# Optimization experiments

Measured on AMD Instinct MI355X. Metric: run time of the kernel, lower is better.

## Reference

```python
import jax, jax.numpy as jnp
import numpy as np
import math

B, S = 4, 1024
V, D, L, H, F, MAXLEN = 32000, 1024, 6, 16, 4096, 2048
DH = D // H
NUM_BUCKETS, MAX_DIST = 32, 256
REL_SCALE = 64.0 ** 0.5
EPS = 1e-5


def setup_inputs() -> dict:
    key = jax.random.key(0)
    ks = iter(jax.random.split(key, 32))
    sd = 0.02
    inp = {
        'src': jax.random.randint(next(ks), (B, S), 0, V),
        'src_mask': jnp.ones((B, 1, 1, S), dtype=jnp.int32),
        'tok_emb': jax.random.normal(next(ks), (V, D), jnp.float32) * sd,
        'pos_emb': jax.random.normal(next(ks), (MAXLEN, D), jnp.float32) * sd,
        'Wq': jax.random.normal(next(ks), (L, D, D), jnp.float32) * sd,
        'bq': jnp.zeros((L, D), jnp.float32),
        'Wk': jax.random.normal(next(ks), (L, D, D), jnp.float32) * sd,
        'bk': jnp.zeros((L, D), jnp.float32),
        'Wv': jax.random.normal(next(ks), (L, D, D), jnp.float32) * sd,
        'bv': jnp.zeros((L, D), jnp.float32),
        'Wo': jax.random.normal(next(ks), (L, D, D), jnp.float32) * sd,
        'bo': jnp.zeros((L, D), jnp.float32),
        'rel_bias': jax.random.normal(next(ks), (L, NUM_BUCKETS, H), jnp.float32) * sd,
        'ln1_g': jnp.ones((L, D), jnp.float32),
        'ln1_b': jnp.zeros((L, D), jnp.float32),
        'W1': jax.random.normal(next(ks), (L, D, F), jnp.float32) * sd,
        'b1': jnp.zeros((L, F), jnp.float32),
        'W2': jax.random.normal(next(ks), (L, F, D), jnp.float32) * sd,
        'b2': jnp.zeros((L, D), jnp.float32),
        'ln2_g': jnp.ones((L, D), jnp.float32),
        'ln2_b': jnp.zeros((L, D), jnp.float32),
    }
    return inp


def _rel_pos_bucket(seq_len):
    # non-causal bucketing (T5-style), matching the torch source
    q = jnp.arange(seq_len)
    k = jnp.arange(seq_len)
    n = q[:, None] - k[None, :]          # == -(k - q)
    nb = NUM_BUCKETS // 2                # 16
    ret = (n < 0).astype(jnp.int32) * nb
    n = jnp.abs(n)
    max_exact = nb // 2                  # 8
    is_small = n < max_exact
    val_large = max_exact + (
        jnp.log(jnp.maximum(n, 1).astype(jnp.float32) / max_exact)
        / math.log(MAX_DIST / max_exact) * (nb - max_exact)
    ).astype(jnp.int32)
    val_large = jnp.minimum(val_large, nb - 1)
    return ret + jnp.where(is_small, n, val_large)  # [S,S] in [0,32)


def _layer_norm(x, g, b):
    mu = jnp.mean(x, axis=-1, keepdims=True)
    var = jnp.var(x, axis=-1, keepdims=True)
    return (x - mu) * jax.lax.rsqrt(var + EPS) * g + b


def reference(src, src_mask, tok_emb, pos_emb, Wq, bq, Wk, bk, Wv, bv, Wo, bo,
              rel_bias, ln1_g, ln1_b, W1, b1, W2, b2, ln2_g, ln2_b):
    seq_len = src.shape[1]
    bucket = _rel_pos_bucket(seq_len)                      # [S,S] int
    x = tok_emb[src] * jnp.sqrt(jnp.float32(D)) + pos_emb[jnp.arange(seq_len)][None]
    scale = jnp.sqrt(jnp.float32(DH))
    neg = jnp.float32(-1e10)

    def layer(x, p):
        (wq, bq_, wk, bk_, wv, bv_, wo, bo_, rb, g1, b1_, w1, bb1, w2, bb2, g2, b2_) = p
        Q = (x @ wq + bq_).reshape(B, seq_len, H, DH)
        K = (x @ wk + bk_).reshape(B, seq_len, H, DH)
        Vv = (x @ wv + bv_).reshape(B, seq_len, H, DH)
        energy = jnp.einsum('bqhd,bkhd->bhqk', Q, K) / scale
        energy = jnp.where(src_mask == 0, neg, energy)
        bias = rb[bucket]                                  # [S,S,H]
        energy = energy + jnp.transpose(bias, (2, 0, 1))[None] * REL_SCALE
        attn = jax.nn.softmax(energy, axis=-1)
        o = jnp.einsum('bhqk,bkhd->bqhd', attn, Vv).reshape(B, seq_len, D)
        o = o @ wo + bo_
        x = _layer_norm(x + o, g1, b1_)
        f = jax.nn.relu(x @ w1 + bb1) @ w2 + bb2
        x = _layer_norm(x + f, g2, b2_)
        return x, None

    params = (Wq, bq, Wk, bk, Wv, bv, Wo, bo, rel_bias,
              ln1_g, ln1_b, W1, b1, W2, b2, ln2_g, ln2_b)
    x, _ = jax.lax.scan(layer, x, params)
    return x
```

## Files before the change

kernel.cpp:

```cpp
#include <hip/hip_runtime.h>

#define B_ 4
#define S_ 1024
#define D_ 1024
#define F_ 4096
#define H_ 16
#define L_ 6
#define M_ (B_*S_)

typedef unsigned short u16;
typedef __attribute__((ext_vector_type(4))) unsigned short u16x4;
typedef __attribute__((ext_vector_type(8))) short s16x8;
typedef __attribute__((ext_vector_type(8))) __bf16 bf16x8;
typedef __attribute__((ext_vector_type(4))) float f32x4;

typedef const __attribute__((address_space(1))) unsigned int gu32;
typedef __attribute__((address_space(3))) unsigned int su32;

__device__ __forceinline__ u16 f2bf(float f) {
  union { float f; unsigned u; } v; v.f = f;
  unsigned u = v.u;
  return (u16)((u + 0x7fffu + ((u >> 16) & 1u)) >> 16);
}

__device__ __forceinline__ f32x4 mfma16(s16x8 a, s16x8 b, f32x4 c) {
  return __builtin_amdgcn_mfma_f32_16x16x32_bf16(
      __builtin_bit_cast(bf16x8, a), __builtin_bit_cast(bf16x8, b), c, 0, 0, 0);
}

__device__ __forceinline__ void gload16(const void* g, void* s) {
  __builtin_amdgcn_global_load_lds((gu32*)g, (su32*)s, 16, 0, 0);
}

template<int OUTMODE>
__device__ __forceinline__ void gemm128_body(
    const u16* __restrict__ A, const u16* __restrict__ Bt,
    const float* __restrict__ bias, float* __restrict__ Cf,
    u16* __restrict__ Ch, int N, int K, int kbeg, int kend,
    const float* __restrict__ bias2, const float* __restrict__ bias3)
{
  __shared__ __align__(16) u16 As[128 * 64];
  __shared__ __align__(16) u16 Bs[128 * 64];
  const int tid = threadIdx.x, lane = tid & 63, w = tid >> 6;
  const int bm = blockIdx.x * 128, bn = blockIdx.y * 128;
  const int wm = (w >> 1) * 64, wn = (w & 1) * 64;

  f32x4 acc[4][4];
#pragma unroll
  for (int i = 0; i < 4; i++)
#pragma unroll
    for (int j = 0; j < 4; j++) acc[i][j] = {0.f, 0.f, 0.f, 0.f};

  for (int k0 = kbeg; k0 < kend; k0 += 64) {
    __syncthreads();
#pragma unroll
    for (int i = 0; i < 4; i++) {
      const int flat = i * 4096 + w * 1024 + lane * 16;
      const int row = flat >> 7, ce = (flat & 127) >> 1;
      gload16(A + (size_t)(bm + row) * K + k0 + ce, As + i * 2048 + w * 512);
      gload16(Bt + (size_t)(bn + row) * K + k0 + ce, Bs + i * 2048 + w * 512);
    }
    __syncthreads();
#pragma unroll
    for (int kk = 0; kk < 2; kk++) {
      s16x8 af[4], bf[4];
#pragma unroll
      for (int mf = 0; mf < 4; mf++)
        af[mf] = *(const s16x8*)&As[(wm + mf * 16 + (lane & 15)) * 64 + kk * 32 + (lane >> 4) * 8];
#pragma unroll
      for (int nf = 0; nf < 4; nf++)
        bf[nf] = *(const s16x8*)&Bs[(wn + nf * 16 + (lane & 15)) * 64 + kk * 32 + (lane >> 4) * 8];
#pragma unroll
      for (int mf = 0; mf < 4; mf++)
#pragma unroll
        for (int nf = 0; nf < 4; nf++)
          acc[mf][nf] = mfma16(af[mf], bf[nf], acc[mf][nf]);
    }
  }
#pragma unroll
  for (int nf = 0; nf < 4; nf++) {
    const int col = bn + wn + nf * 16 + (lane & 15);
    float bvv = 0.f, sc = 1.0f;
    int zz = 0, lc = col;
    if (OUTMODE == 3) {
      zz = col >> 10; lc = col & 1023;
      const float* bp = (zz == 0) ? bias : (zz == 1) ? bias2 : bias3;
      bvv = bp[lc];
      sc = (zz == 0) ? 0.125f : 1.0f;
    }
#pragma unroll
    for (int mf = 0; mf < 4; mf++) {
#pragma unroll
      for (int j = 0; j < 4; j++) {
        const int row = bm + wm + mf * 16 + ((lane >> 4) << 2) + j;
        const float v = acc[mf][nf][j];
        if (OUTMODE == 0) {
          Cf[(size_t)row * N + col] = v;
        } else {
          Ch[(size_t)zz * M_ * D_ + (size_t)row * D_ + lc] = f2bf((v + bvv) * sc);
        }
      }
    }
  }
}

__global__ __launch_bounds__(256, 3) void gemm_qkvf(
    const u16* __restrict__ A, const u16* __restrict__ WT,
    const float* __restrict__ bq, const float* __restrict__ bk,
    const float* __restrict__ bv, u16* __restrict__ Out)
{
  gemm128_body<3>(A, WT, bq, nullptr, Out, 3 * D_, D_, 0, D_, bk, bv);
}

__global__ __launch_bounds__(256, 3) void gemm_splitk2(
    const u16* __restrict__ A, const u16* __restrict__ WT,
    float* __restrict__ P, int N, int K)
{
  const int z = blockIdx.z;
  const int half = K >> 1;
  gemm128_body<0>(A, WT, nullptr, P + (size_t)z * M_ * (size_t)N, nullptr,
                  N, K, z * half, z * half + half, nullptr, nullptr);
}

__device__ __forceinline__ s16x8 readfrag(const u16* half, int r, int kk, int hi4) {
  const int c = (kk * 64 + hi4 * 16) ^ ((r & 7) << 4);
  return *(const s16x8*)((const char*)half + r * 128 + c);
}

__device__ __forceinline__ void stage_half(
    const u16* __restrict__ src, int ldk, u16* lds_half, int w, int lane)
{
#pragma unroll
  for (int j = 0; j < 2; j++) {
    const int flat = j * 8192 + w * 1024 + lane * 16;
    const int row = flat >> 7;
    const int kb = (flat & 127) ^ ((row & 7) << 4);
    gload16(src + (size_t)row * ldk + (kb >> 1), lds_half + j * 4096 + w * 512);
  }
}

#define BAR     asm volatile("s_barrier" ::: "memory")
#define PH_PRE  asm volatile("s_barrier" ::: "memory"); __builtin_amdgcn_s_setprio(1)
#define PH_POST __builtin_amdgcn_s_setprio(0); __builtin_amdgcn_sched_barrier(0)
#define VM4     asm volatile("s_waitcnt vmcnt(4)" ::: "memory")
#define VM0     asm volatile("s_waitcnt vmcnt(0)" ::: "memory")

#define READ_B(bufhalf) do { \
  _Pragma("unroll") for (int nf = 0; nf < 4; nf++) \
  _Pragma("unroll") for (int kk = 0; kk < 2; kk++) \
    bfr[nf][kk] = readfrag(bufhalf, rb0 + nf * 16 + lo16, kk, hi4); } while (0)
#define READ_A(bufhalf, Q) do { \
  _Pragma("unroll") for (int m = 0; m < 2; m++) \
  _Pragma("unroll") for (int kk = 0; kk < 2; kk++) \
    af[m][kk] = readfrag(bufhalf, (2 * (Q) + m) * 16 + lo16, kk, hi4); } while (0)
#define DO_MFMA(Q) do { \
  _Pragma("unroll") for (int kk = 0; kk < 2; kk++) \
  _Pragma("unroll") for (int m = 0; m < 2; m++) \
  _Pragma("unroll") for (int nf = 0; nf < 4; nf++) \
    acc[2 * (Q) + m][nf] = mfma16(af[m][kk], bfr[nf][kk], acc[2 * (Q) + m][nf]); } while (0)

__global__ __launch_bounds__(512, 2) void gemm_ffn1(
    const u16* __restrict__ A, const u16* __restrict__ Bt,
    const float* __restrict__ bias, u16* __restrict__ Ch)
{
  __shared__ __align__(16) u16 As[2][2][8192];
  __shared__ __align__(16) u16 Bs[2][2][8192];
  const int tid = threadIdx.x, lane = tid & 63, w = tid >> 6;
  const int wr = w >> 2, wc = w & 3;
  const int lo16 = lane & 15, hi4 = lane >> 4;
  const int bm = blockIdx.x * 256, bn = blockIdx.y * 256;
  const int rb0 = (wc & 1) * 64;
  const int K = D_, N = F_;

  const u16* Abase = A + (size_t)bm * K;
  const u16* Bbase = Bt + (size_t)bn * K;
  const size_t h1 = (size_t)128 * K;
  const int NT = K >> 6, NI = NT >> 1;

  f32x4 acc[8][4];
#pragma unroll
  for (int i = 0; i < 8; i++)
#pragma unroll
    for (int j = 0; j < 4; j++) acc[i][j] = {0.f, 0.f, 0.f, 0.f};

  stage_half(Abase,           K, As[0][0], w, lane);
  stage_half(Abase + h1,      K, As[0][1], w, lane);
  stage_half(Bbase,           K, Bs[0][0], w, lane);
  stage_half(Bbase + h1,      K, Bs[0][1], w, lane);
  stage_half(Abase + 64,      K, As[1][0], w, lane);
  stage_half(Abase + h1 + 64, K, As[1][1], w, lane);
  stage_half(Bbase + 64,      K, Bs[1][0], w, lane);
  stage_half(Bbase + h1 + 64, K, Bs[1][1], w, lane);
  asm volatile("s_waitcnt vmcnt(8)" ::: "memory");
  BAR;

  const u16* Ae = As[0][wr]; const u16* Ao = As[1][wr];
  const u16* Be = Bs[0][wc >> 1]; const u16* Bo = Bs[1][wc >> 1];
  s16x8 af[2][2], bfr[4][2];

  for (int it = 0; it < NI - 1; ++it) {
    READ_B(Be); READ_A(Ae, 0);
    if (it > 0) {
      stage_half(Abase +      (size_t)(2 * it + 1) * 64, K, As[1][0], w, lane);
      stage_half(Abase + h1 + (size_t)(2 * it + 1) * 64, K, As[1][1], w, lane);
    }
    PH_PRE; DO_MFMA(0); PH_POST; BAR;
    READ_A(Ae, 1);
    stage_half(Bbase +      (size_t)(2 * it + 2) * 64, K, Bs[0][0], w, lane);
    PH_PRE; DO_MFMA(1); PH_POST; BAR;
    READ_A(Ae, 2);
    stage_half(Bbase + h1 + (size_t)(2 * it + 2) * 64, K, Bs[0][1], w, lane);
    PH_PRE; DO_MFMA(2); PH_POST; BAR;
    READ_A(Ae, 3);
    PH_PRE; DO_MFMA(3); PH_POST; VM4; BAR;
    READ_B(Bo); READ_A(Ao, 0);
    stage_half(Abase +      (size_t)(2 * it + 2) * 64, K, As[0][0], w, lane);
    stage_half(Abase + h1 + (size_t)(2 * it + 2) * 64, K, As[0][1], w, lane);
    PH_PRE; DO_MFMA(0); PH_POST; BAR;
    READ_A(Ao, 1);
    stage_half(Bbase +      (size_t)(2 * it + 3) * 64, K, Bs[1][0], w, lane);
    PH_PRE; DO_MFMA(1); PH_POST; BAR;
    READ_A(Ao, 2);
    stage_half(Bbase + h1 + (size_t)(2 * it + 3) * 64, K, Bs[1][1], w, lane);
    PH_PRE; DO_MFMA(2); PH_POST; BAR;
    READ_A(Ao, 3);
    PH_PRE; DO_MFMA(3); PH_POST; VM4; BAR;
  }
  READ_B(Be); READ_A(Ae, 0);
  stage_half(Abase +      (size_t)(NT - 1) * 64, K, As[1][0], w, lane);
  stage_half(Abase + h1 + (size_t)(NT - 1) * 64, K, As[1][1], w, lane);
  PH_PRE; DO_MFMA(0); PH_POST; BAR;
  READ_A(Ae, 1);             PH_PRE; DO_MFMA(1); PH_POST; BAR;
  READ_A(Ae, 2);             PH_PRE; DO_MFMA(2); PH_POST; BAR;
  READ_A(Ae, 3);             PH_PRE; DO_MFMA(3); PH_POST; VM0; BAR;
  READ_B(Bo); READ_A(Ao, 0); PH_PRE; DO_MFMA(0); PH_POST; BAR;
  READ_A(Ao, 1);             PH_PRE; DO_MFMA(1); PH_POST; BAR;
  READ_A(Ao, 2);             PH_PRE; DO_MFMA(2); PH_POST; BAR;
  READ_A(Ao, 3);             PH_PRE; DO_MFMA(3); PH_POST;

  const int row0 = bm + wr * 128, col0 = bn + wc * 64;
#pragma unroll
  for (int nf = 0; nf < 4; nf++) {
    const int col = col0 + nf * 16 + lo16;
    const float bv = bias[col];
#pragma unroll
    for (int mf = 0; mf < 8; mf++) {
#pragma unroll
      for (int j = 0; j < 4; j++) {
        const int row = row0 + mf * 16 + hi4 * 4 + j;
        Ch[(size_t)row * N + col] = f2bf(fmaxf(acc[mf][nf][j] + bv, 0.f));
      }
    }
  }
}

__global__ __launch_bounds__(256) void transpose_cvt(
    const float* __restrict__ src, u16* __restrict__ dst, int R, int Cc)
{
  __shared__ float t[32][33];
  const int c0 = blockIdx.x * 32, r0 = blockIdx.y * 32;
  const int tx = threadIdx.x & 31, ty = threadIdx.x >> 5;
#pragma unroll
  for (int i = 0; i < 4; i++)
    t[ty + 8 * i][tx] = src[(size_t)(r0 + ty + 8 * i) * Cc + c0 + tx];
  __syncthreads();
#pragma unroll
  for (int i = 0; i < 4; i++)
    dst[(size_t)(c0 + ty + 8 * i) * R + r0 + tx] = f2bf(t[tx][ty + 8 * i]);
}

__global__ __launch_bounds__(256) void transpose4(
    const float* __restrict__ Wq, const float* __restrict__ Wk,
    const float* __restrict__ Wv, const float* __restrict__ Wo,
    u16* __restrict__ WTqkv, u16* __restrict__ WTo)
{
  __shared__ float t[32][33];
  const int z = blockIdx.z;
  const float* src = (z == 0) ? Wq : (z == 1) ? Wk : (z == 2) ? Wv : Wo;
  u16* dst = (z < 3) ? WTqkv + (size_t)z * D_ * D_ : WTo;
  const int c0 = blockIdx.x * 32, r0 = blockIdx.y * 32;
  const int tx = threadIdx.x & 31, ty = threadIdx.x >> 5;
#pragma unroll
  for (int i = 0; i < 4; i++)
    t[ty + 8 * i][tx] = src[(size_t)(r0 + ty + 8 * i) * D_ + c0 + tx];
  __syncthreads();
#pragma unroll
  for (int i = 0; i < 4; i++)
    dst[(size_t)(c0 + ty + 8 * i) * D_ + r0 + tx] = f2bf(t[tx][ty + 8 * i]);
}

__global__ __launch_bounds__(256) void vt_transpose(
    const u16* __restrict__ Vb, u16* __restrict__ Vt)
{
  __shared__ u16 t[64][66];
  const int s0 = blockIdx.x * 64;
  const int bh = blockIdx.y;
  const int b = bh >> 4, h = bh & 15;
  const int tid = threadIdx.x;
  const int row = tid >> 2;
  const int c0 = (tid & 3) * 16;
  const u16* src = Vb + (size_t)(b * S_ + s0 + row) * D_ + h * 64 + c0;
  *(s16x8*)&t[row][c0] = *(const s16x8*)src;
  *(s16x8*)&t[row][c0 + 8] = *(const s16x8*)(src + 8);
  __syncthreads();
  const int dh = tid >> 2;
  const int sc = (tid & 3) * 16;
  s16x8 a, bv;
#pragma unroll
  for (int u = 0; u < 8; u++) a[u] = (short)t[sc + u][dh];
#pragma unroll
  for (int u = 0; u < 8; u++) bv[u] = (short)t[sc + 8 + u][dh];
  u16* dst = Vt + (size_t)(bh * 64 + dh) * S_ + s0 + sc;
  *(s16x8*)dst = a;
  *(s16x8*)(dst + 8) = bv;
}

__device__ __forceinline__ s16x8 lds_swz(const u16* base, int row, int cb) {
  const int addr = row * 128 + (cb ^ ((row & 7) << 4));
  return *(const s16x8*)((const char*)base + addr);
}

__global__ __launch_bounds__(256, 4) void attn_kernel(
    const u16* __restrict__ Qb, const u16* __restrict__ Kb,
    const u16* __restrict__ Vt, const int* __restrict__ mask,
    const float* __restrict__ rb, u16* __restrict__ AO)
{
  __shared__ float lut[2048];
  __shared__ __align__(16) u16 Ks[64 * 64];
  __shared__ __align__(16) u16 Vs[64 * 64];
  __shared__ __align__(16) u16 Ps[4][16 * 68];

  const int tid = threadIdx.x;
  const int lane = tid & 63;
  const int w = tid >> 6;
  const int bh = blockIdx.x;
  const int b = bh >> 4, h = bh & 15;
  const int q0 = blockIdx.y * 64 + w * 16;
  const int bS = b * S_, hh = h * 64;

  for (int idx = tid; idx < 2048; idx += 256) {
    const int rel = idx - 1024;
    const int ret = rel < 0 ? 16 : 0;
    const int n = rel < 0 ? -rel : rel;
    int bu;
    if (n < 8) bu = ret + n;
    else {
      const float t = logf((float)n * 0.125f) * (8.0f / 3.4657359027997265f);
      int vl = 8 + (int)t;
      if (vl > 15) vl = 15;
      bu = ret + vl;
    }
    lut[idx] = rb[bu * 16 + h] * 8.0f;
  }

  s16x8 qf[2];
#pragma unroll
  for (int kk = 0; kk < 2; kk++)
    qf[kk] = *(const s16x8*)(Qb + (size_t)(bS + q0 + (lane & 15)) * D_ + hh +
                             kk * 32 + (lane >> 4) * 8);

  f32x4 oacc[4];
#pragma unroll
  for (int i = 0; i < 4; i++) oacc[i] = {0.f, 0.f, 0.f, 0.f};
  float rm[4], rl[4];
#pragma unroll
  for (int j = 0; j < 4; j++) { rm[j] = -3e38f; rl[j] = 0.f; }

  for (int kt = 0; kt < S_; kt += 64) {
    __syncthreads();
#pragma unroll
    for (int i = 0; i < 2; i++) {
      const int flat = i * 4096 + w * 1024 + lane * 16;
      const int row = flat >> 7;
      const int ce = ((flat & 127) ^ ((row & 7) << 4)) >> 1;
      gload16(Kb + (size_t)(bS + kt + row) * D_ + hh + ce, Ks + i * 2048 + w * 512);
      gload16(Vt + (size_t)(bh * 64 + row) * S_ + kt + ce, Vs + i * 2048 + w * 512);
    }
    __syncthreads();

    f32x4 sacc[4];
#pragma unroll
    for (int i = 0; i < 4; i++) sacc[i] = {0.f, 0.f, 0.f, 0.f};
#pragma unroll
    for (int kk = 0; kk < 2; kk++) {
      const int cb = kk * 64 + (lane >> 4) * 16;
#pragma unroll
      for (int nf = 0; nf < 4; nf++) {
        const s16x8 kb = lds_swz(Ks, nf * 16 + (lane & 15), cb);
        sacc[nf] = mfma16(qf[kk], kb, sacc[nf]);
      }
    }

    int km[4];
#pragma unroll
    for (int nf = 0; nf < 4; nf++)
      km[nf] = mask[bS + kt + nf * 16 + (lane & 15)];

    const int lidx0 = q0 + (lane >> 4) * 4 + 1024 - kt - (lane & 15);
#pragma unroll
    for (int j = 0; j < 4; j++) {
      const int lrow = ((lane >> 4) << 2) + j;
      float sc[4];
      float mx = -3e38f;
#pragma unroll
      for (int nf = 0; nf < 4; nf++) {
        float s = (km[nf] == 0) ? -1e10f : sacc[nf][j];
        s += lut[lidx0 + j - nf * 16];
        sc[nf] = s;
        mx = fmaxf(mx, s);
      }
      mx = fmaxf(mx, __shfl_xor(mx, 1));
      mx = fmaxf(mx, __shfl_xor(mx, 2));
      mx = fmaxf(mx, __shfl_xor(mx, 4));
      mx = fmaxf(mx, __shfl_xor(mx, 8));
      const float m_new = fmaxf(rm[j], mx);
      const float fs = __expf(rm[j] - m_new);
      rm[j] = m_new;
      float psum = 0.f;
#pragma unroll
      for (int nf = 0; nf < 4; nf++) {
        const float p = __expf(sc[nf] - m_new);
        psum += p;
        Ps[w][lrow * 68 + nf * 16 + (lane & 15)] = f2bf(p);
      }
      psum += __shfl_xor(psum, 1);
      psum += __shfl_xor(psum, 2);
      psum += __shfl_xor(psum, 4);
      psum += __shfl_xor(psum, 8);
      rl[j] = rl[j] * fs + psum;
#pragma unroll
      for (int df = 0; df < 4; df++) oacc[df][j] *= fs;
    }

#pragma unroll
    for (int kk = 0; kk < 2; kk++) {
      const s16x8 pa = *(const s16x8*)&Ps[w][(lane & 15) * 68 + kk * 32 + (lane >> 4) * 8];
      const int cb = kk * 64 + (lane >> 4) * 16;
#pragma unroll
      for (int df = 0; df < 4; df++) {
        const s16x8 vb = lds_swz(Vs, df * 16 + (lane & 15), cb);
        oacc[df] = mfma16(pa, vb, oacc[df]);
      }
    }
  }

  float inv[4];
#pragma unroll
  for (int j = 0; j < 4; j++) inv[j] = 1.0f / rl[j];
#pragma unroll
  for (int df = 0; df < 4; df++)
#pragma unroll
    for (int j = 0; j < 4; j++) {
      const int qrow = q0 + ((lane >> 4) << 2) + j;
      AO[(size_t)(bS + qrow) * D_ + hh + df * 16 + (lane & 15)] =
          f2bf(oacc[df][j] * inv[j]);
    }
}

__global__ __launch_bounds__(256) void ln_fused2(
    const float* __restrict__ X, const float* __restrict__ P0,
    const float* __restrict__ P1, const float* __restrict__ bias,
    const float* __restrict__ g, const float* __restrict__ be,
    float* __restrict__ Yf, u16* __restrict__ Yh)
{
  const int row = blockIdx.x;
  const int tid = threadIdx.x;
  const size_t off = (size_t)row * D_;
  const float4 xv = ((const float4*)(X + off))[tid];
  const float4 p0 = ((const float4*)(P0 + off))[tid];
  const float4 p1 = ((const float4*)(P1 + off))[tid];
  const float4 bb = ((const float4*)bias)[tid];
  const float v0 = xv.x + p0.x + p1.x + bb.x;
  const float v1 = xv.y + p0.y + p1.y + bb.y;
  const float v2 = xv.z + p0.z + p1.z + bb.z;
  const float v3 = xv.w + p0.w + p1.w + bb.w;
  float sum = v0 + v1 + v2 + v3;
  float ss = v0 * v0 + v1 * v1 + v2 * v2 + v3 * v3;
#pragma unroll
  for (int o = 1; o < 64; o <<= 1) {
    sum += __shfl_xor(sum, o);
    ss += __shfl_xor(ss, o);
  }
  __shared__ float s1[4], s2[4];
  if ((tid & 63) == 0) { s1[tid >> 6] = sum; s2[tid >> 6] = ss; }
  __syncthreads();
  sum = s1[0] + s1[1] + s1[2] + s1[3];
  ss = s2[0] + s2[1] + s2[2] + s2[3];
  const float mu = sum * (1.f / D_);
  const float var = ss * (1.f / D_) - mu * mu;
  const float rstd = rsqrtf(var + 1e-5f);
  const float4 gv = ((const float4*)g)[tid];
  const float4 bv = ((const float4*)be)[tid];
  float4 y;
  y.x = (v0 - mu) * rstd * gv.x + bv.x;
  y.y = (v1 - mu) * rstd * gv.y + bv.y;
  y.z = (v2 - mu) * rstd * gv.z + bv.z;
  y.w = (v3 - mu) * rstd * gv.w + bv.w;
  ((float4*)(Yf + off))[tid] = y;
  u16x4 hv;
  hv.x = f2bf(y.x); hv.y = f2bf(y.y); hv.z = f2bf(y.z); hv.w = f2bf(y.w);
  ((u16x4*)(Yh + off))[tid] = hv;
}

__global__ __launch_bounds__(256) void embed_kernel(
    const int* __restrict__ src, const float* __restrict__ tok,
    const float* __restrict__ pos, float* __restrict__ X, u16* __restrict__ Xh)
{
  const int row = blockIdx.x;
  const int s = row & (S_ - 1);
  const int t = src[row];
  const int tid = threadIdx.x;
  const float4 tv = ((const float4*)(tok + (size_t)t * D_))[tid];
  const float4 pv = ((const float4*)(pos + (size_t)s * D_))[tid];
  float4 y;
  y.x = tv.x * 32.f + pv.x;
  y.y = tv.y * 32.f + pv.y;
  y.z = tv.z * 32.f + pv.z;
  y.w = tv.w * 32.f + pv.w;
  ((float4*)(X + (size_t)row * D_))[tid] = y;
  u16x4 hv;
  hv.x = f2bf(y.x); hv.y = f2bf(y.y); hv.z = f2bf(y.z); hv.w = f2bf(y.w);
  ((u16x4*)(Xh + (size_t)row * D_))[tid] = hv;
}

extern "C" void kernel_launch(void* const* d_in, const int* in_sizes, int n_in,
                              void* d_out, int out_size, void* d_ws, size_t ws_size,
                              hipStream_t stream)
{
  const int* src = (const int*)d_in[0];
  const int* mask = (const int*)d_in[1];
  const float* tok_emb = (const float*)d_in[2];
  const float* pos_emb = (const float*)d_in[3];
  const float* Wq = (const float*)d_in[4];
  const float* bq = (const float*)d_in[5];
  const float* Wk = (const float*)d_in[6];
  const float* bk = (const float*)d_in[7];
  const float* Wv = (const float*)d_in[8];
  const float* bv = (const float*)d_in[9];
  const float* Wo = (const float*)d_in[10];
  const float* bo = (const float*)d_in[11];
  const float* rb = (const float*)d_in[12];
  const float* g1 = (const float*)d_in[13];
  const float* b1n = (const float*)d_in[14];
  const float* W1 = (const float*)d_in[15];
  const float* b1f = (const float*)d_in[16];
  const float* W2 = (const float*)d_in[17];
  const float* b2f = (const float*)d_in[18];
  const float* g2 = (const float*)d_in[19];
  const float* b2n = (const float*)d_in[20];
  float* out = (float*)d_out;

  char* ws = (char*)d_ws;
  const size_t MB = 1ull << 20;
  float* xb   = (float*)(ws + 0);
  u16*   xb16 = (u16*)(ws + 16 * MB);
  u16*   Qb16 = (u16*)(ws + 24 * MB);
  u16*   Kb16 = (u16*)(ws + 32 * MB);
  u16*   Vb16 = (u16*)(ws + 40 * MB);
  u16*   Vt16 = (u16*)(ws + 48 * MB);
  u16*   AO16 = (u16*)(ws + 56 * MB);
  float* Pp   = (float*)(ws + 64 * MB);
  u16*   WTqkv= (u16*)(ws + 96 * MB);
  u16*   WTo  = (u16*)(ws + 102 * MB);
  u16*   WT1  = (u16*)(ws + 104 * MB);
  u16*   WT2  = (u16*)(ws + 112 * MB);
  u16*   Hb16 = (u16*)(ws + 24 * MB);

  embed_kernel<<<M_, 256, 0, stream>>>(src, tok_emb, pos_emb, xb, xb16);

  for (int l = 0; l < L_; l++) {
    const size_t oDD = (size_t)l * D_ * D_;
    const size_t oDF = (size_t)l * D_ * F_;

    transpose4<<<dim3(32, 32, 4), 256, 0, stream>>>(
        Wq + oDD, Wk + oDD, Wv + oDD, Wo + oDD, WTqkv, WTo);
    transpose_cvt<<<dim3(F_ / 32, D_ / 32), 256, 0, stream>>>(W1 + oDF, WT1, D_, F_);
    transpose_cvt<<<dim3(D_ / 32, F_ / 32), 256, 0, stream>>>(W2 + oDF, WT2, F_, D_);

    gemm_qkvf<<<dim3(M_ / 128, 3 * D_ / 128), 256, 0, stream>>>(
        xb16, WTqkv, bq + l * D_, bk + l * D_, bv + l * D_, Qb16);

    vt_transpose<<<dim3(S_ / 64, B_ * H_), 256, 0, stream>>>(Vb16, Vt16);

    attn_kernel<<<dim3(B_ * H_, S_ / 64), 256, 0, stream>>>(
        Qb16, Kb16, Vt16, mask, rb + l * 32 * H_, AO16);

    gemm_splitk2<<<dim3(M_ / 128, D_ / 128, 2), 256, 0, stream>>>(
        AO16, WTo, Pp, D_, D_);

    ln_fused2<<<M_, 256, 0, stream>>>(
        xb, Pp, Pp + (size_t)M_ * D_, bo + l * D_,
        g1 + l * D_, b1n + l * D_, xb, xb16);

    gemm_ffn1<<<dim3(M_ / 256, F_ / 256), 512, 0, stream>>>(
        xb16, WT1, b1f + l * F_, Hb16);

    gemm_splitk2<<<dim3(M_ / 128, D_ / 128, 2), 256, 0, stream>>>(
        Hb16, WT2, Pp, D_, F_);

    ln_fused2<<<M_, 256, 0, stream>>>(
        xb, Pp, Pp + (size_t)M_ * D_, b2f + l * D_,
        g2 + l * D_, b2n + l * D_, (l == L_ - 1) ? out : xb, xb16);
  }
}
```

Before: 1.515 ms.

## Use bf16 residual and split-K partials, 256-tile FFN2, double-buffer attention KV

```diff
diff --git a/kernel.cpp b/kernel.cpp
--- a/kernel.cpp
+++ b/kernel.cpp
@@ -22,6 +22,9 @@
   unsigned u = v.u;
   return (u16)((u + 0x7fffu + ((u >> 16) & 1u)) >> 16);
 }
+__device__ __forceinline__ float bf2f(u16 h) {
+  union { unsigned u; float f; } v; v.u = (unsigned)h << 16; return v.f;
+}
 
 __device__ __forceinline__ f32x4 mfma16(s16x8 a, s16x8 b, f32x4 c) {
   return __builtin_amdgcn_mfma_f32_16x16x32_bf16(
@@ -35,9 +38,9 @@
 template<int OUTMODE>
 __device__ __forceinline__ void gemm128_body(
     const u16* __restrict__ A, const u16* __restrict__ Bt,
-    const float* __restrict__ bias, float* __restrict__ Cf,
-    u16* __restrict__ Ch, int N, int K, int kbeg, int kend,
-    const float* __restrict__ bias2, const float* __restrict__ bias3)
+    const float* __restrict__ b0, const float* __restrict__ b1,
+    const float* __restrict__ b2, u16* __restrict__ Ch,
+    int N, int K, int kbeg, int kend)
 {
   __shared__ __align__(16) u16 As[128 * 64];
   __shared__ __align__(16) u16 Bs[128 * 64];
@@ -84,7 +87,7 @@
     int zz = 0, lc = col;
     if (OUTMODE == 3) {
       zz = col >> 10; lc = col & 1023;
-      const float* bp = (zz == 0) ? bias : (zz == 1) ? bias2 : bias3;
+      const float* bp = (zz == 0) ? b0 : (zz == 1) ? b1 : b2;
       bvv = bp[lc];
       sc = (zz == 0) ? 0.125f : 1.0f;
     }
@@ -94,8 +97,8 @@
       for (int j = 0; j < 4; j++) {
         const int row = bm + wm + mf * 16 + ((lane >> 4) << 2) + j;
         const float v = acc[mf][nf][j];
-        if (OUTMODE == 0) {
-          Cf[(size_t)row * N + col] = v;
+        if (OUTMODE == 1) {
+          Ch[(size_t)row * N + col] = f2bf(v);
         } else {
           Ch[(size_t)zz * M_ * D_ + (size_t)row * D_ + lc] = f2bf((v + bvv) * sc);
         }
@@ -109,17 +112,16 @@
     const float* __restrict__ bq, const float* __restrict__ bk,
     const float* __restrict__ bv, u16* __restrict__ Out)
 {
-  gemm128_body<3>(A, WT, bq, nullptr, Out, 3 * D_, D_, 0, D_, bk, bv);
-}
-
-__global__ __launch_bounds__(256, 3) void gemm_splitk2(
+  gemm128_body<3>(A, WT, bq, bk, bv, Out, 3 * D_, D_, 0, D_);
+}
+
+__global__ __launch_bounds__(256, 3) void gemm_osplit2(
     const u16* __restrict__ A, const u16* __restrict__ WT,
-    float* __restrict__ P, int N, int K)
+    u16* __restrict__ P)
 {
   const int z = blockIdx.z;
-  const int half = K >> 1;
-  gemm128_body<0>(A, WT, nullptr, P + (size_t)z * M_ * (size_t)N, nullptr,
-                  N, K, z * half, z * half + half, nullptr, nullptr);
+  gemm128_body<1>(A, WT, nullptr, nullptr, nullptr,
+                  P + (size_t)z * M_ * D_, D_, D_, z * 512, z * 512 + 512);
 }
 
 __device__ __forceinline__ s16x8 readfrag(const u16* half, int r, int kk, int hi4) {
@@ -159,9 +161,11 @@
   _Pragma("unroll") for (int nf = 0; nf < 4; nf++) \
     acc[2 * (Q) + m][nf] = mfma16(af[m][kk], bfr[nf][kk], acc[2 * (Q) + m][nf]); } while (0)
 
-__global__ __launch_bounds__(512, 2) void gemm_ffn1(
+template<int OUTMODE>
+__device__ __forceinline__ void gemm256_body(
     const u16* __restrict__ A, const u16* __restrict__ Bt,
-    const float* __restrict__ bias, u16* __restrict__ Ch)
+    const float* __restrict__ bias, u16* __restrict__ Ch,
+    int N, int K, int kbeg, int kslice)
 {
   __shared__ __align__(16) u16 As[2][2][8192];
   __shared__ __align__(16) u16 Bs[2][2][8192];
@@ -170,12 +174,11 @@
   const int lo16 = lane & 15, hi4 = lane >> 4;
   const int bm = blockIdx.x * 256, bn = blockIdx.y * 256;
   const int rb0 = (wc & 1) * 64;
-  const int K = D_, N = F_;
-
-  const u16* Abase = A + (size_t)bm * K;
-  const u16* Bbase = Bt + (size_t)bn * K;
+
+  const u16* Abase = A + (size_t)bm * K + kbeg;
+  const u16* Bbase = Bt + (size_t)bn * K + kbeg;
   const size_t h1 = (size_t)128 * K;
-  const int NT = K >> 6, NI = NT >> 1;
+  const int NT = kslice >> 6, NI = NT >> 1;
 
   f32x4 acc[8][4];
 #pragma unroll
@@ -242,16 +245,34 @@
 #pragma unroll
   for (int nf = 0; nf < 4; nf++) {
     const int col = col0 + nf * 16 + lo16;
-    const float bv = bias[col];
+    const float bv = (OUTMODE == 2) ? bias[col] : 0.f;
 #pragma unroll
     for (int mf = 0; mf < 8; mf++) {
 #pragma unroll
       for (int j = 0; j < 4; j++) {
         const int row = row0 + mf * 16 + hi4 * 4 + j;
-        Ch[(size_t)row * N + col] = f2bf(fmaxf(acc[mf][nf][j] + bv, 0.f));
+        float v = acc[mf][nf][j];
+        if (OUTMODE == 2) v = fmaxf(v + bv, 0.f);
+        Ch[(size_t)row * N + col] = f2bf(v);
       }
     }
   }
+}
+
+__global__ __launch_bounds__(512, 2) void gemm_ffn1(
+    const u16* __restrict__ A, const u16* __restrict__ WT,
+    const float* __restrict__ bias, u16* __restrict__ Out)
+{
+  gemm256_body<2>(A, WT, bias, Out, F_, D_, 0, D_);
+}
+
+__global__ __launch_bounds__(512, 2) void gemm_ffn2sp4(
+    const u16* __restrict__ A, const u16* __restrict__ WT,
+    u16* __restrict__ P)
+{
+  const int z = blockIdx.z;
+  gemm256_body<4>(A, WT, nullptr, P + (size_t)z * M_ * D_,
+                  D_, F_, z * 1024, 1024);
 }
 
 __global__ __launch_bounds__(256) void transpose_cvt(
@@ -320,14 +341,24 @@
   return *(const s16x8*)((const char*)base + addr);
 }
 
-__global__ __launch_bounds__(256, 4) void attn_kernel(
+#define ATTN_STAGE(t, buf) do { \
+  const int kt2 = (t) * 64; \
+  _Pragma("unroll") for (int i2 = 0; i2 < 2; i2++) { \
+    const int flat2 = i2 * 4096 + w * 1024 + lane * 16; \
+    const int row2 = flat2 >> 7; \
+    const int ce2 = ((flat2 & 127) ^ ((row2 & 7) << 4)) >> 1; \
+    gload16(Kb + (size_t)(bS + kt2 + row2) * D_ + hh + ce2, Ks[buf] + i2 * 2048 + w * 512); \
+    gload16(Vt + (size_t)(bh * 64 + row2) * S_ + kt2 + ce2, Vs[buf] + i2 * 2048 + w * 512); \
+  } } while (0)
+
+__global__ __launch_bounds__(256, 3) void attn_kernel(
     const u16* __restrict__ Qb, const u16* __restrict__ Kb,
     const u16* __restrict__ Vt, const int* __restrict__ mask,
     const float* __restrict__ rb, u16* __restrict__ AO)
 {
   __shared__ float lut[2048];
-  __shared__ __align__(16) u16 Ks[64 * 64];
-  __shared__ __align__(16) u16 Vs[64 * 64];
+  __shared__ __align__(16) u16 Ks[2][64 * 64];
+  __shared__ __align__(16) u16 Vs[2][64 * 64];
   __shared__ __align__(16) u16 Ps[4][16 * 68];
 
   const int tid = threadIdx.x;
@@ -337,6 +368,7 @@
   const int b = bh >> 4, h = bh & 15;
   const int q0 = blockIdx.y * 64 + w * 16;
   const int bS = b * S_, hh = h * 64;
+  const int lo16 = lane & 15, hi4 = lane >> 4;
 
   for (int idx = tid; idx < 2048; idx += 256) {
     const int rel = idx - 1024;
@@ -356,8 +388,8 @@
   s16x8 qf[2];
 #pragma unroll
   for (int kk = 0; kk < 2; kk++)
-    qf[kk] = *(const s16x8*)(Qb + (size_t)(bS + q0 + (lane & 15)) * D_ + hh +
-                             kk * 32 + (lane >> 4) * 8);
+    qf[kk] = *(const s16x8*)(Qb + (size_t)(bS + q0 + lo16) * D_ + hh +
+                             kk * 32 + hi4 * 8);
 
   f32x4 oacc[4];
 #pragma unroll
@@ -366,27 +398,24 @@
 #pragma unroll
   for (int j = 0; j < 4; j++) { rm[j] = -3e38f; rl[j] = 0.f; }
 
-  for (int kt = 0; kt < S_; kt += 64) {
-    __syncthreads();
-#pragma unroll
-    for (int i = 0; i < 2; i++) {
-      const int flat = i * 4096 + w * 1024 + lane * 16;
-      const int row = flat >> 7;
-      const int ce = ((flat & 127) ^ ((row & 7) << 4)) >> 1;
-      gload16(Kb + (size_t)(bS + kt + row) * D_ + hh + ce, Ks + i * 2048 + w * 512);
-      gload16(Vt + (size_t)(bh * 64 + row) * S_ + kt + ce, Vs + i * 2048 + w * 512);
-    }
-    __syncthreads();
+  ATTN_STAGE(0, 0);
+  asm volatile("s_waitcnt vmcnt(0) lgkmcnt(0)" ::: "memory");
+  __builtin_amdgcn_s_barrier();
+
+  for (int t = 0; t < S_ / 64; ++t) {
+    const int cur = t & 1;
+    const int kt = t * 64;
+    if (t < S_ / 64 - 1) ATTN_STAGE(t + 1, cur ^ 1);
 
     f32x4 sacc[4];
 #pragma unroll
     for (int i = 0; i < 4; i++) sacc[i] = {0.f, 0.f, 0.f, 0.f};
 #pragma unroll
     for (int kk = 0; kk < 2; kk++) {
-      const int cb = kk * 64 + (lane >> 4) * 16;
+      const int cb = kk * 64 + hi4 * 16;
 #pragma unroll
       for (int nf = 0; nf < 4; nf++) {
-        const s16x8 kb = lds_swz(Ks, nf * 16 + (lane & 15), cb);
+        const s16x8 kb = lds_swz(Ks[cur], nf * 16 + lo16, cb);
         sacc[nf] = mfma16(qf[kk], kb, sacc[nf]);
       }
     }
@@ -394,12 +423,12 @@
     int km[4];
 #pragma unroll
     for (int nf = 0; nf < 4; nf++)
-      km[nf] = mask[bS + kt + nf * 16 + (lane & 15)];
-
-    const int lidx0 = q0 + (lane >> 4) * 4 + 1024 - kt - (lane & 15);
+      km[nf] = mask[bS + kt + nf * 16 + lo16];
+
+    const int lidx0 = q0 + hi4 * 4 + 1024 - kt - lo16;
 #pragma unroll
     for (int j = 0; j < 4; j++) {
-      const int lrow = ((lane >> 4) << 2) + j;
+      const int lrow = (hi4 << 2) + j;
       float sc[4];
       float mx = -3e38f;
 #pragma unroll
@@ -413,35 +442,40 @@
       mx = fmaxf(mx, __shfl_xor(mx, 2));
       mx = fmaxf(mx, __shfl_xor(mx, 4));
       mx = fmaxf(mx, __shfl_xor(mx, 8));
-      const float m_new = fmaxf(rm[j], mx);
-      const float fs = __expf(rm[j] - m_new);
-      rm[j] = m_new;
+      if (mx > rm[j] + 8.f) {
+        const float fs = __expf(rm[j] - mx);
+        rm[j] = mx;
+        rl[j] *= fs;
+#pragma unroll
+        for (int df = 0; df < 4; df++) oacc[df][j] *= fs;
+      }
       float psum = 0.f;
 #pragma unroll
       for (int nf = 0; nf < 4; nf++) {
-        const float p = __expf(sc[nf] - m_new);
+        const float p = __expf(sc[nf] - rm[j]);
         psum += p;
-        Ps[w][lrow * 68 + nf * 16 + (lane & 15)] = f2bf(p);
+        Ps[w][lrow * 68 + nf * 16 + lo16] = f2bf(p);
       }
       psum += __shfl_xor(psum, 1);
       psum += __shfl_xor(psum, 2);
       psum += __shfl_xor(psum, 4);
       psum += __shfl_xor(psum, 8);
-      rl[j] = rl[j] * fs + psum;
-#pragma unroll
-      for (int df = 0; df < 4; df++) oacc[df][j] *= fs;
+      rl[j] += psum;
     }
 
 #pragma unroll
     for (int kk = 0; kk < 2; kk++) {
-      const s16x8 pa = *(const s16x8*)&Ps[w][(lane & 15) * 68 + kk * 32 + (lane >> 4) * 8];
-      const int cb = kk * 64 + (lane >> 4) * 16;
+      const s16x8 pa = *(const s16x8*)&Ps[w][lo16 * 68 + kk * 32 + hi4 * 8];
+      const int cb = kk * 64 + hi4 * 16;
 #pragma unroll
       for (int df = 0; df < 4; df++) {
-        const s16x8 vb = lds_swz(Vs, df * 16 + (lane & 15), cb);
+        const s16x8 vb = lds_swz(Vs[cur], df * 16 + lo16, cb);
         oacc[df] = mfma16(pa, vb, oacc[df]);
       }
     }
+
+    asm volatile("s_waitcnt vmcnt(0)" ::: "memory");
+    __builtin_amdgcn_s_barrier();
   }
 
   float inv[4];
@@ -451,31 +485,37 @@
   for (int df = 0; df < 4; df++)
 #pragma unroll
     for (int j = 0; j < 4; j++) {
-      const int qrow = q0 + ((lane >> 4) << 2) + j;
-      AO[(size_t)(bS + qrow) * D_ + hh + df * 16 + (lane & 15)] =
+      const int qrow = q0 + (hi4 << 2) + j;
+      AO[(size_t)(bS + qrow) * D_ + hh + df * 16 + lo16] =
           f2bf(oacc[df][j] * inv[j]);
     }
 }
 
-__global__ __launch_bounds__(256) void ln_fused2(
-    const float* __restrict__ X, const float* __restrict__ P0,
-    const float* __restrict__ P1, const float* __restrict__ bias,
-    const float* __restrict__ g, const float* __restrict__ be,
-    float* __restrict__ Yf, u16* __restrict__ Yh)
+template<int NP>
+__global__ __launch_bounds__(256) void ln_fusedb(
+    const u16* __restrict__ Xh, const u16* __restrict__ P,
+    const float* __restrict__ bias, const float* __restrict__ g,
+    const float* __restrict__ be, u16* __restrict__ Yh, float* __restrict__ Yf)
 {
   const int row = blockIdx.x;
   const int tid = threadIdx.x;
   const size_t off = (size_t)row * D_;
-  const float4 xv = ((const float4*)(X + off))[tid];
-  const float4 p0 = ((const float4*)(P0 + off))[tid];
-  const float4 p1 = ((const float4*)(P1 + off))[tid];
+  const size_t ps = (size_t)M_ * D_;
+  const u16x4 xv = ((const u16x4*)(Xh + off))[tid];
+  float v[4];
+#pragma unroll
+  for (int q = 0; q < 4; q++) v[q] = bf2f(xv[q]);
+#pragma unroll
+  for (int p = 0; p < NP; p++) {
+    const u16x4 pv = ((const u16x4*)(P + p * ps + off))[tid];
+#pragma unroll
+    for (int q = 0; q < 4; q++) v[q] += bf2f(pv[q]);
+  }
   const float4 bb = ((const float4*)bias)[tid];
-  const float v0 = xv.x + p0.x + p1.x + bb.x;
-  const float v1 = xv.y + p0.y + p1.y + bb.y;
-  const float v2 = xv.z + p0.z + p1.z + bb.z;
-  const float v3 = xv.w + p0.w + p1.w + bb.w;
-  float sum = v0 + v1 + v2 + v3;
-  float ss = v0 * v0 + v1 * v1 + v2 * v2 + v3 * v3;
+  v[0] += bb.x; v[1] += bb.y; v[2] += bb.z; v[3] += bb.w;
+
+  float sum = v[0] + v[1] + v[2] + v[3];
+  float ss = v[0] * v[0] + v[1] * v[1] + v[2] * v[2] + v[3] * v[3];
 #pragma unroll
   for (int o = 1; o < 64; o <<= 1) {
     sum += __shfl_xor(sum, o);
@@ -491,20 +531,23 @@
   const float rstd = rsqrtf(var + 1e-5f);
   const float4 gv = ((const float4*)g)[tid];
   const float4 bv = ((const float4*)be)[tid];
-  float4 y;
-  y.x = (v0 - mu) * rstd * gv.x + bv.x;
-  y.y = (v1 - mu) * rstd * gv.y + bv.y;
-  y.z = (v2 - mu) * rstd * gv.z + bv.z;
-  y.w = (v3 - mu) * rstd * gv.w + bv.w;
-  ((float4*)(Yf + off))[tid] = y;
+  float y[4];
+  y[0] = (v[0] - mu) * rstd * gv.x + bv.x;
+  y[1] = (v[1] - mu) * rstd * gv.y + bv.y;
+  y[2] = (v[2] - mu) * rstd * gv.z + bv.z;
+  y[3] = (v[3] - mu) * rstd * gv.w + bv.w;
   u16x4 hv;
-  hv.x = f2bf(y.x); hv.y = f2bf(y.y); hv.z = f2bf(y.z); hv.w = f2bf(y.w);
+  hv.x = f2bf(y[0]); hv.y = f2bf(y[1]); hv.z = f2bf(y[2]); hv.w = f2bf(y[3]);
   ((u16x4*)(Yh + off))[tid] = hv;
+  if (Yf != nullptr) {
+    float4 yf; yf.x = y[0]; yf.y = y[1]; yf.z = y[2]; yf.w = y[3];
+    ((float4*)(Yf + off))[tid] = yf;
+  }
 }
 
 __global__ __launch_bounds__(256) void embed_kernel(
     const int* __restrict__ src, const float* __restrict__ tok,
-    const float* __restrict__ pos, float* __restrict__ X, u16* __restrict__ Xh)
+    const float* __restrict__ pos, u16* __restrict__ Xh)
 {
   const int row = blockIdx.x;
   const int s = row & (S_ - 1);
@@ -512,14 +555,11 @@
   const int tid = threadIdx.x;
   const float4 tv = ((const float4*)(tok + (size_t)t * D_))[tid];
   const float4 pv = ((const float4*)(pos + (size_t)s * D_))[tid];
-  float4 y;
-  y.x = tv.x * 32.f + pv.x;
-  y.y = tv.y * 32.f + pv.y;
-  y.z = tv.z * 32.f + pv.z;
-  y.w = tv.w * 32.f + pv.w;
-  ((float4*)(X + (size_t)row * D_))[tid] = y;
   u16x4 hv;
-  hv.x = f2bf(y.x); hv.y = f2bf(y.y); hv.z = f2bf(y.z); hv.w = f2bf(y.w);
+  hv.x = f2bf(tv.x * 32.f + pv.x);
+  hv.y = f2bf(tv.y * 32.f + pv.y);
+  hv.z = f2bf(tv.z * 32.f + pv.z);
+  hv.w = f2bf(tv.w * 32.f + pv.w);
   ((u16x4*)(Xh + (size_t)row * D_))[tid] = hv;
 }
 
@@ -552,21 +592,20 @@
 
   char* ws = (char*)d_ws;
   const size_t MB = 1ull << 20;
-  float* xb   = (float*)(ws + 0);
-  u16*   xb16 = (u16*)(ws + 16 * MB);
-  u16*   Qb16 = (u16*)(ws + 24 * MB);
-  u16*   Kb16 = (u16*)(ws + 32 * MB);
-  u16*   Vb16 = (u16*)(ws + 40 * MB);
-  u16*   Vt16 = (u16*)(ws + 48 * MB);
-  u16*   AO16 = (u16*)(ws + 56 * MB);
-  float* Pp   = (float*)(ws + 64 * MB);
-  u16*   WTqkv= (u16*)(ws + 96 * MB);
-  u16*   WTo  = (u16*)(ws + 102 * MB);
-  u16*   WT1  = (u16*)(ws + 104 * MB);
-  u16*   WT2  = (u16*)(ws + 112 * MB);
-  u16*   Hb16 = (u16*)(ws + 24 * MB);
-
-  embed_kernel<<<M_, 256, 0, stream>>>(src, tok_emb, pos_emb, xb, xb16);
+  u16* xb16  = (u16*)(ws + 0);
+  u16* Qb16  = (u16*)(ws + 8 * MB);
+  u16* Kb16  = (u16*)(ws + 16 * MB);
+  u16* Vb16  = (u16*)(ws + 24 * MB);
+  u16* Vt16  = (u16*)(ws + 32 * MB);
+  u16* AO16  = (u16*)(ws + 40 * MB);
+  u16* Pp16  = (u16*)(ws + 48 * MB);
+  u16* WTqkv = (u16*)(ws + 80 * MB);
+  u16* WTo   = (u16*)(ws + 86 * MB);
+  u16* WT1   = (u16*)(ws + 88 * MB);
+  u16* WT2   = (u16*)(ws + 96 * MB);
+  u16* Hb16  = (u16*)(ws + 8 * MB);
+
+  embed_kernel<<<M_, 256, 0, stream>>>(src, tok_emb, pos_emb, xb16);
 
   for (int l = 0; l < L_; l++) {
     const size_t oDD = (size_t)l * D_ * D_;
@@ -585,21 +624,20 @@
     attn_kernel<<<dim3(B_ * H_, S_ / 64), 256, 0, stream>>>(
         Qb16, Kb16, Vt16, mask, rb + l * 32 * H_, AO16);
 
-    gemm_splitk2<<<dim3(M_ / 128, D_ / 128, 2), 256, 0, stream>>>(
-        AO16, WTo, Pp, D_, D_);
-
-    ln_fused2<<<M_, 256, 0, stream>>>(
-        xb, Pp, Pp + (size_t)M_ * D_, bo + l * D_,
-        g1 + l * D_, b1n + l * D_, xb, xb16);
+    gemm_osplit2<<<dim3(M_ / 128, D_ / 128, 2), 256, 0, stream>>>(
+        AO16, WTo, Pp16);
+
+    ln_fusedb<2><<<M_, 256, 0, stream>>>(
+        xb16, Pp16, bo + l * D_, g1 + l * D_, b1n + l * D_, xb16, nullptr);
 
     gemm_ffn1<<<dim3(M_ / 256, F_ / 256), 512, 0, stream>>>(
         xb16, WT1, b1f + l * F_, Hb16);
 
-    gemm_splitk2<<<dim3(M_ / 128, D_ / 128, 2), 256, 0, stream>>>(
-        Hb16, WT2, Pp, D_, F_);
-
-    ln_fused2<<<M_, 256, 0, stream>>>(
-        xb, Pp, Pp + (size_t)M_ * D_, b2f + l * D_,
-        g2 + l * D_, b2n + l * D_, (l == L_ - 1) ? out : xb, xb16);
-  }
-}
+    gemm_ffn2sp4<<<dim3(M_ / 256, D_ / 256, 4), 512, 0, stream>>>(
+        Hb16, WT2, Pp16);
+
+    ln_fusedb<4><<<M_, 256, 0, stream>>>(
+        xb16, Pp16, b2f + l * D_, g2 + l * D_, b2n + l * D_, xb16,
+        (l == L_ - 1) ? out : nullptr);
+  }
+}
```

Result: slower. 1.572 ms (+3.8%).
